# Kernel tuning notes

Hardware: AMD Instinct MI355X
Metric: run time of the kernel (lower is better)

Reference implementation:

```python
import jax, jax.numpy as jnp
import numpy as np


def setup_inputs() -> dict:
    key = jax.random.key(0)
    k1, k2 = jax.random.split(key)
    B, C, H, W = 1, 3, 3500, 2500
    src = jax.random.normal(k1, (B, C, H, W), dtype=jnp.float32)
    flow = jax.random.normal(k2, (B, 2, H, W), dtype=jnp.float32)
    return {"src": src, "flow": flow}


def reference(src, flow):
    """SpatialTransformer.forward: flow + identity grid -> normalize -> bilinear
    grid_sample (zeros padding, align_corners=True). Returns (warped, norm_grid).
    src:  [B, C, H, W] float
    flow: [B, 2, H, W] float; channel 0 = x (width) displacement, channel 1 = y.
    """
    B, C, H, W = src.shape
    dt = flow.dtype
    xs = jnp.arange(W, dtype=dt)  # identity x coords
    ys = jnp.arange(H, dtype=dt)  # identity y coords
    gx = flow[:, 0] + xs[None, None, :]  # [B, H, W] absolute x coord
    gy = flow[:, 1] + ys[None, :, None]  # [B, H, W] absolute y coord
    # normalize to [-1, 1]; max_extent = (W-1, H-1) per torch code
    nx = 2.0 * gx / (W - 1) - 1.0
    ny = 2.0 * gy / (H - 1) - 1.0
    norm_grid = jnp.stack([nx, ny], axis=-1)  # [B, H, W, 2], second output

    # grid_sample with align_corners=True: unnormalize back to pixel coords
    ix = (nx + 1.0) * 0.5 * (W - 1)
    iy = (ny + 1.0) * 0.5 * (H - 1)
    x0 = jnp.floor(ix)
    y0 = jnp.floor(iy)
    x1 = x0 + 1.0
    y1 = y0 + 1.0
    wx1 = ix - x0
    wx0 = 1.0 - wx1
    wy1 = iy - y0
    wy0 = 1.0 - wy1

    def gather(xi, yi):
        # zeros padding: out-of-range corners contribute 0
        valid = (xi >= 0) & (xi <= W - 1) & (yi >= 0) & (yi <= H - 1)
        xc = jnp.clip(xi, 0, W - 1).astype(jnp.int32)
        yc = jnp.clip(yi, 0, H - 1).astype(jnp.int32)
        vals = jax.vmap(lambda sb, yb, xb: sb[:, yb, xb])(src, yc, xc)  # [B,C,H,W]
        return vals * valid.astype(src.dtype)[:, None]

    out = (gather(x0, y0) * (wx0 * wy0)[:, None]
           + gather(x1, y0) * (wx1 * wy0)[:, None]
           + gather(x0, y1) * (wx0 * wy1)[:, None]
           + gather(x1, y1) * (wx1 * wy1)[:, None])
    return out, norm_grid
```

## Files before the change

### kernel.cpp

```cpp
#include <hip/hip_runtime.h>

#define HH 3500
#define WW 2500
#define TXs 64
#define TYs 16
#define WIN_H 32
#define WIN_W 84
#define WIN_W4 (WIN_W/4)
#define NTX ((WW + TXs - 1)/TXs)
#define NTY ((HH + TYs - 1)/TYs)
#define NXCD 8

typedef float f32x4 __attribute__((ext_vector_type(4)));

__global__ __launch_bounds__(256, 5) void st_warp_v4(
    const float* __restrict__ src,
    const float* __restrict__ flow,
    float* __restrict__ out)
{
    __shared__ float sm[3][WIN_H][WIN_W];

    const int nwg = NTX * NTY;
    const int cpx = nwg / NXCD;
    const int bid = blockIdx.x;
    const int sbid = (bid % NXCD) * cpx + bid / NXCD;
    const int xt = sbid / NTY;
    const int yt = sbid - xt * NTY;

    const int tx0 = xt * TXs;
    const int ty0 = yt * TYs;
    const int cx0 = tx0 - 8;
    const int ry0 = ty0 - 8;

    const long HW = (long)HH * WW;
    const int tid = threadIdx.x;

    const bool colsafe = (cx0 >= 0) && (cx0 + WIN_W <= WW);
    if (colsafe) {
#pragma unroll
        for (int e0 = 0; e0 < 3*WIN_H*WIN_W4; e0 += 256) {
            const int e = e0 + tid;
            if (e < 3*WIN_H*WIN_W4) {
                const int c   = e / (WIN_H*WIN_W4);
                const int rem = e - c*(WIN_H*WIN_W4);
                const int r   = rem / WIN_W4;
                const int v   = rem - r*WIN_W4;
                int gy = ry0 + r; gy = min(max(gy, 0), HH-1);
                const f32x4 val = *reinterpret_cast<const f32x4*>(
                    src + (long)c*HW + (long)gy*WW + (cx0 + 4*v));
                *reinterpret_cast<f32x4*>(&sm[c][r][4*v]) = val;
            }
        }
    } else {
        for (int e = tid; e < 3*WIN_H*WIN_W; e += 256) {
            const int c   = e / (WIN_H*WIN_W);
            const int rem = e - c*(WIN_H*WIN_W);
            const int r   = rem / WIN_W;
            const int j   = rem - r*WIN_W;
            int gy = ry0 + r; gy = min(max(gy, 0), HH-1);
            int gx = cx0 + j; gx = min(max(gx, 0), WW-1);
            sm[c][r][j] = src[(long)c*HW + (long)gy*WW + gx];
        }
    }
    __syncthreads();

    const int r  = tid >> 4;
    const int xb = tx0 + (tid & 15) * 4;
    const int y  = ty0 + r;
    if (xb >= WW || y >= HH) return;

    const long idx = (long)y * WW + xb;
    const f32x4 fx4 = *reinterpret_cast<const f32x4*>(flow + idx);
    const f32x4 fy4 = *reinterpret_cast<const f32x4*>(flow + HW + idx);

    float o[3][4];
    float ngv[8];

#pragma unroll
    for (int k = 0; k < 4; ++k) {
        const int x = xb + k;
        const float gx = fx4[k] + (float)x;
        const float gy = fy4[k] + (float)y;

        const float nx = 2.0f * gx / (float)(WW-1) - 1.0f;
        const float ny = 2.0f * gy / (float)(HH-1) - 1.0f;
        ngv[2*k]   = nx;
        ngv[2*k+1] = ny;

        const float ixp = (nx + 1.0f) * 0.5f * (float)(WW-1);
        const float iyp = (ny + 1.0f) * 0.5f * (float)(HH-1);

        const float x0f = floorf(ixp), y0f = floorf(iyp);
        const float wx1 = ixp - x0f, wx0 = 1.0f - wx1;
        const float wy1 = iyp - y0f, wy0 = 1.0f - wy1;

        const int x0 = (int)x0f, y0i = (int)y0f;
        const int x1 = x0 + 1,  y1i = y0i + 1;

        const bool vx0 = (x0  >= 0) & (x0  < WW);
        const bool vx1 = (x1  >= 0) & (x1  < WW);
        const bool vy0 = (y0i >= 0) & (y0i < HH);
        const bool vy1 = (y1i >= 0) & (y1i < HH);

        const float w00 = wx0*wy0*((vx0 & vy0) ? 1.0f : 0.0f);
        const float w10 = wx1*wy0*((vx1 & vy0) ? 1.0f : 0.0f);
        const float w01 = wx0*wy1*((vx0 & vy1) ? 1.0f : 0.0f);
        const float w11 = wx1*wy1*((vx1 & vy1) ? 1.0f : 0.0f);

        const int x0c = min(max(x0,  0), WW-1);
        const int x1c = min(max(x1,  0), WW-1);
        const int y0c = min(max(y0i, 0), HH-1);
        const int y1c = min(max(y1i, 0), HH-1);

        const bool inwin = (x0 >= cx0) & (x1 <= cx0 + WIN_W - 1) &
                           (y0i >= ry0) & (y1i <= ry0 + WIN_H - 1);

        if (inwin) {
            const int lx0 = x0c - cx0, lx1 = x1c - cx0;
            const int ly0 = y0c - ry0, ly1 = y1c - ry0;
#pragma unroll
            for (int c = 0; c < 3; ++c) {
                o[c][k] = sm[c][ly0][lx0]*w00 + sm[c][ly0][lx1]*w10
                        + sm[c][ly1][lx0]*w01 + sm[c][ly1][lx1]*w11;
            }
        } else {
            const long off00 = (long)y0c*WW + x0c;
            const long off10 = (long)y0c*WW + x1c;
            const long off01 = (long)y1c*WW + x0c;
            const long off11 = (long)y1c*WW + x1c;
#pragma unroll
            for (int c = 0; c < 3; ++c) {
                const float* __restrict__ s = src + (long)c*HW;
                o[c][k] = s[off00]*w00 + s[off10]*w10
                        + s[off01]*w01 + s[off11]*w11;
            }
        }
    }

#pragma unroll
    for (int c = 0; c < 3; ++c) {
        f32x4 v = {o[c][0], o[c][1], o[c][2], o[c][3]};
        __builtin_nontemporal_store(v, reinterpret_cast<f32x4*>(out + (long)c*HW + idx));
    }
    float* ngbase = out + 3*HW + 2*idx;
    f32x4 n0 = {ngv[0], ngv[1], ngv[2], ngv[3]};
    f32x4 n1 = {ngv[4], ngv[5], ngv[6], ngv[7]};
    __builtin_nontemporal_store(n0, reinterpret_cast<f32x4*>(ngbase));
    __builtin_nontemporal_store(n1, reinterpret_cast<f32x4*>(ngbase + 4));
}

extern "C" void kernel_launch(void* const* d_in, const int* in_sizes, int n_in,
                              void* d_out, int out_size, void* d_ws, size_t ws_size,
                              hipStream_t stream) {
    const float* src  = (const float*)d_in[0];
    const float* flow = (const float*)d_in[1];
    float* out = (float*)d_out;
    (void)d_ws; (void)ws_size; (void)in_sizes; (void)n_in; (void)out_size;

    dim3 block(256, 1, 1);
    dim3 grid(NTX * NTY, 1, 1);
    st_warp_v4<<<grid, block, 0, stream>>>(src, flow, out);
}
```

Before: 113.3 us.

## Drop shared-memory source window; gather bilinear taps directly from global memory

Removes the per-block LDS staging of a 3x32x84 source window, along with its __syncthreads, and reads all four bilinear corners straight from global memory, relying on L1/L2 caching for locality. It also replaces the nontemporal output stores with ordinary stores and drops the occupancy hint from the launch bounds. This removes the LDS fill cost, the barrier, the branch divergence and the LDS occupancy limit, in exchange for more global/L1 gather traffic per output pixel.

Measured after the change: 157.9 us. 39.4% more time.

```diff
diff --git a/kernel.cpp b/kernel.cpp
--- a/kernel.cpp
+++ b/kernel.cpp
@@ -4,22 +4,17 @@
 #define WW 2500
 #define TXs 64
 #define TYs 16
-#define WIN_H 32
-#define WIN_W 84
-#define WIN_W4 (WIN_W/4)
 #define NTX ((WW + TXs - 1)/TXs)
 #define NTY ((HH + TYs - 1)/TYs)
 #define NXCD 8
 
 typedef float f32x4 __attribute__((ext_vector_type(4)));
 
-__global__ __launch_bounds__(256, 5) void st_warp_v4(
+__global__ __launch_bounds__(256) void st_warp_v5(
     const float* __restrict__ src,
     const float* __restrict__ flow,
     float* __restrict__ out)
 {
-    __shared__ float sm[3][WIN_H][WIN_W];
-
     const int nwg = NTX * NTY;
     const int cpx = nwg / NXCD;
     const int bid = blockIdx.x;
@@ -29,40 +24,9 @@
 
     const int tx0 = xt * TXs;
     const int ty0 = yt * TYs;
-    const int cx0 = tx0 - 8;
-    const int ry0 = ty0 - 8;
 
     const long HW = (long)HH * WW;
     const int tid = threadIdx.x;
-
-    const bool colsafe = (cx0 >= 0) && (cx0 + WIN_W <= WW);
-    if (colsafe) {
-#pragma unroll
-        for (int e0 = 0; e0 < 3*WIN_H*WIN_W4; e0 += 256) {
-            const int e = e0 + tid;
-            if (e < 3*WIN_H*WIN_W4) {
-                const int c   = e / (WIN_H*WIN_W4);
-                const int rem = e - c*(WIN_H*WIN_W4);
-                const int r   = rem / WIN_W4;
-                const int v   = rem - r*WIN_W4;
-                int gy = ry0 + r; gy = min(max(gy, 0), HH-1);
-                const f32x4 val = *reinterpret_cast<const f32x4*>(
-                    src + (long)c*HW + (long)gy*WW + (cx0 + 4*v));
-                *reinterpret_cast<f32x4*>(&sm[c][r][4*v]) = val;
-            }
-        }
-    } else {
-        for (int e = tid; e < 3*WIN_H*WIN_W; e += 256) {
-            const int c   = e / (WIN_H*WIN_W);
-            const int rem = e - c*(WIN_H*WIN_W);
-            const int r   = rem / WIN_W;
-            const int j   = rem - r*WIN_W;
-            int gy = ry0 + r; gy = min(max(gy, 0), HH-1);
-            int gx = cx0 + j; gx = min(max(gx, 0), WW-1);
-            sm[c][r][j] = src[(long)c*HW + (long)gy*WW + gx];
-        }
-    }
-    __syncthreads();
 
     const int r  = tid >> 4;
     const int xb = tx0 + (tid & 15) * 4;
@@ -112,41 +76,29 @@
         const int y0c = min(max(y0i, 0), HH-1);
         const int y1c = min(max(y1i, 0), HH-1);
 
-        const bool inwin = (x0 >= cx0) & (x1 <= cx0 + WIN_W - 1) &
-                           (y0i >= ry0) & (y1i <= ry0 + WIN_H - 1);
+        const long off00 = (long)y0c*WW + x0c;
+        const long off10 = (long)y0c*WW + x1c;
+        const long off01 = (long)y1c*WW + x0c;
+        const long off11 = (long)y1c*WW + x1c;
 
-        if (inwin) {
-            const int lx0 = x0c - cx0, lx1 = x1c - cx0;
-            const int ly0 = y0c - ry0, ly1 = y1c - ry0;
 #pragma unroll
-            for (int c = 0; c < 3; ++c) {
-                o[c][k] = sm[c][ly0][lx0]*w00 + sm[c][ly0][lx1]*w10
-                        + sm[c][ly1][lx0]*w01 + sm[c][ly1][lx1]*w11;
-            }
-        } else {
-            const long off00 = (long)y0c*WW + x0c;
-            const long off10 = (long)y0c*WW + x1c;
-            const long off01 = (long)y1c*WW + x0c;
-            const long off11 = (long)y1c*WW + x1c;
-#pragma unroll
-            for (int c = 0; c < 3; ++c) {
-                const float* __restrict__ s = src + (long)c*HW;
-                o[c][k] = s[off00]*w00 + s[off10]*w10
-                        + s[off01]*w01 + s[off11]*w11;
-            }
+        for (int c = 0; c < 3; ++c) {
+            const float* __restrict__ s = src + (long)c*HW;
+            o[c][k] = s[off00]*w00 + s[off10]*w10
+                    + s[off01]*w01 + s[off11]*w11;
         }
     }
 
 #pragma unroll
     for (int c = 0; c < 3; ++c) {
         f32x4 v = {o[c][0], o[c][1], o[c][2], o[c][3]};
-        __builtin_nontemporal_store(v, reinterpret_cast<f32x4*>(out + (long)c*HW + idx));
+        *reinterpret_cast<f32x4*>(out + (long)c*HW + idx) = v;
     }
     float* ngbase = out + 3*HW + 2*idx;
     f32x4 n0 = {ngv[0], ngv[1], ngv[2], ngv[3]};
     f32x4 n1 = {ngv[4], ngv[5], ngv[6], ngv[7]};
-    __builtin_nontemporal_store(n0, reinterpret_cast<f32x4*>(ngbase));
-    __builtin_nontemporal_store(n1, reinterpret_cast<f32x4*>(ngbase + 4));
+    *reinterpret_cast<f32x4*>(ngbase)     = n0;
+    *reinterpret_cast<f32x4*>(ngbase + 4) = n1;
 }
 
 extern "C" void kernel_launch(void* const* d_in, const int* in_sizes, int n_in,
@@ -159,5 +111,5 @@
 
     dim3 block(256, 1, 1);
     dim3 grid(NTX * NTY, 1, 1);
-    st_warp_v4<<<grid, block, 0, stream>>>(src, flow, out);
+    st_warp_v5<<<grid, block, 0, stream>>>(src, flow, out);
 }
```
